# Performance work log

Measured on AMD Instinct MI355X. Metric: run time of the kernel, lower is better.

Reference implementation:

```python
import jax, jax.numpy as jnp
import numpy as np

NS = 100000; NT = 100000; M = 512; D = 256; DL = 128; H = 4; C = 256; K = 64
ITERS = 50; POS_MARGIN = 0.1


def conv1(w, b, x):
    # 1x1 Conv1d: x (B, Cin, N), w (Cout, Cin)
    return jnp.einsum('oi,bin->bon', w, x) + b[None, :, None]


def attn_block(p, x, src):
    # attentional propagation: MHA message + MLP([x, msg]) (residual added by caller)
    wq, bq, wk, bk, wv, bv, wm, bm, w1, b1, w2, b2 = p
    B, Dm, N = x.shape
    Dh = Dm // H
    Nm = src.shape[2]
    q = conv1(wq, bq, x).reshape(B, H, Dh, N)
    k = conv1(wk, bk, src).reshape(B, H, Dh, Nm)
    v = conv1(wv, bv, src).reshape(B, H, Dh, Nm)
    a = jax.nn.softmax(jnp.einsum('bhdn,bhdm->bhnm', q, k) * (1.0 / np.sqrt(Dh)), axis=-1)
    msg = jnp.einsum('bhnm,bhdm->bhdn', a, v).reshape(B, Dm, N)
    msg = conv1(wm, bm, msg)
    h = jax.nn.relu(conv1(w1, b1, jnp.concatenate([x, msg], axis=1)))
    return conv1(w2, b2, h)


def nn_id(points, nodes):
    # 1-NN node id per point; points (N,3), nodes (M,3)
    d = (jnp.sum(points * points, 1, keepdims=True) - 2.0 * points @ nodes.T
         + jnp.sum(nodes * nodes, 1)[None, :])
    return jnp.argmin(d, axis=1)


def build_patches(pcd_id, m, k):
    # grouping_wrapper: first k point indices assigned to each node, -1 padded
    n = pcd_id.shape[0]
    order = jnp.argsort(pcd_id)  # stable
    sid = pcd_id[order]
    starts = jnp.searchsorted(sid, jnp.arange(m))
    rank = jnp.arange(n) - starts[sid]
    patch = jnp.full((m, k), -1, jnp.int32)
    patch = patch.at[sid, rank].set(order.astype(jnp.int32), mode='drop')  # rank>=k dropped
    mask = (patch < 0).astype(jnp.float32)
    return jnp.where(patch < 0, 0, patch), mask


def log_optimal_transport(scores, alpha, iters):
    b, m, n = scores.shape
    bins0 = jnp.full((b, m, 1), alpha)
    bins1 = jnp.full((b, 1, n), alpha)
    corner = jnp.full((b, 1, 1), alpha)
    Z = jnp.concatenate([jnp.concatenate([scores, bins0], 2),
                         jnp.concatenate([bins1, corner], 2)], 1)
    norm = -np.log(m + n)
    log_mu = jnp.concatenate([jnp.full((m,), norm, jnp.float32), jnp.array([np.log(n) + norm], jnp.float32)])
    log_nu = jnp.concatenate([jnp.full((n,), norm, jnp.float32), jnp.array([np.log(m) + norm], jnp.float32)])
    log_mu = jnp.broadcast_to(log_mu, (b, m + 1))
    log_nu = jnp.broadcast_to(log_nu, (b, n + 1))

    def body(carry, _):
        u, v = carry
        u = log_mu - jax.nn.logsumexp(Z + v[:, None, :], axis=2)
        v = log_nu - jax.nn.logsumexp(Z + u[:, :, None], axis=1)
        return (u, v), None

    (u, v), _ = jax.lax.scan(body, (jnp.zeros((b, m + 1)), jnp.zeros((b, n + 1))), None, length=iters)
    return Z + u[:, :, None] + v[:, None, :] - norm


def rpmnet_sinkhorn(log_alpha, bins0, bins1, iters):
    b = log_alpha.shape[0]
    corner = jnp.zeros((b, 1, 1), log_alpha.dtype)
    la = jnp.concatenate([jnp.concatenate([log_alpha, bins0], 2),
                          jnp.concatenate([bins1, corner], 2)], 1)

    def body(la, _):
        row = la - jax.nn.logsumexp(la, axis=2, keepdims=True)
        la = jnp.concatenate([row[:, :-1, :], la[:, -1:, :]], axis=1)  # normalize all rows but slack
        col = la - jax.nn.logsumexp(la, axis=1, keepdims=True)
        la = jnp.concatenate([col[:, :, :-1], la[:, :, -1:]], axis=2)  # normalize all cols but slack
        return la, None

    la, _ = jax.lax.scan(body, la, None, length=iters)
    return la


def _forward(src_pcd_c, tgt_pcd_c, src_node_c, tgt_node_c, src_feats_c, tgt_feats_c,
             src_final_f, tgt_final_f, rot, trans, src_pcd_raw, tgt_pcd_raw,
             c_wq, c_bq, c_wk, c_bk, c_wv, c_bv, c_wm, c_bm, c_w1, c_b1, c_w2, c_b2,
             l_wq, l_bq, l_wk, l_bk, l_wv, l_bv, l_wm, l_bm, l_w1, l_b1, l_w2, l_b2,
             fp_w, fp_b, lfp_w, lfp_b, bin_score, node_corr):
    # KNN assignment + patch grouping (irregular gather/scatter)
    src_patch, src_mask = build_patches(nn_id(src_pcd_c, src_node_c), M, K)
    tgt_patch, tgt_mask = build_patches(nn_id(tgt_pcd_c, tgt_node_c), M, K)
    # coarse attention stack (self, cross, self) with residuals
    cp = lambda i: (c_wq[i], c_bq[i], c_wk[i], c_bk[i], c_wv[i], c_bv[i], c_wm[i], c_bm[i],
                    c_w1[i], c_b1[i], c_w2[i], c_b2[i])
    sf, tf = src_feats_c, tgt_feats_c
    sf = sf + attn_block(cp(0), sf, sf); tf = tf + attn_block(cp(0), tf, tf)
    sf = sf + attn_block(cp(1), sf, tf); tf = tf + attn_block(cp(1), tf, sf)  # sequential, like torch
    sf = sf + attn_block(cp(2), sf, sf); tf = tf + attn_block(cp(2), tf, tf)
    sf = conv1(fp_w, fp_b, sf); tf = conv1(fp_w, fp_b, tf)
    scores = jnp.einsum('bdn,bdm->bnm', sf, tf) / np.sqrt(D)
    scores = log_optimal_transport(scores, bin_score, ITERS)
    # correspondence-driven patch gather
    sn = node_corr[:, 0]; tn = node_corr[:, 1]
    src_sel = src_patch[sn].reshape(-1)
    tgt_sel = tgt_patch[tn].reshape(-1)
    smask = src_mask[sn]; tmask = tgt_mask[tn]  # (C,K)
    # GT local scores (training path)
    src_raw_t = (rot @ src_pcd_raw.T + trans).T
    sc = src_raw_t[src_sel].reshape(C, K, 3)
    tc = tgt_pcd_raw[tgt_sel].reshape(C, K, 3)
    d2 = jnp.maximum(jnp.sum(sc * sc, -1)[:, :, None] + jnp.sum(tc * tc, -1)[:, None, :]
                     - 2.0 * jnp.einsum('cnd,cmd->cnm', sc, tc), 0.0)
    gt = (jnp.sqrt(d2) < POS_MARGIN).astype(jnp.float32)
    row = jnp.maximum(1.0 - jnp.sum(gt, -1), 0.0)[:, :, None]
    col = jnp.maximum(1.0 - jnp.sum(gt, -2), 0.0)[:, None, :]
    col = jnp.concatenate([col, jnp.zeros((C, 1, 1), jnp.float32)], -1)
    gt = jnp.concatenate([jnp.concatenate([gt, row], -1), col], -2)  # (C,K+1,K+1)
    gt = gt.at[:, :-1, :].multiply(1.0 - smask[:, :, None])
    gt = gt.at[:, :, :-1].multiply(1.0 - tmask[:, None, :])
    # local patch features + attention stack
    spf = src_final_f[src_sel].reshape(C, K, DL).transpose(0, 2, 1)  # (C,DL,K)
    tpf = tgt_final_f[tgt_sel].reshape(C, K, DL).transpose(0, 2, 1)
    lp = lambda i: (l_wq[i], l_bq[i], l_wk[i], l_bk[i], l_wv[i], l_bv[i], l_wm[i], l_bm[i],
                    l_w1[i], l_b1[i], l_w2[i], l_b2[i])
    spf = spf + attn_block(lp(0), spf, spf); tpf = tpf + attn_block(lp(0), tpf, tpf)
    spf = spf + attn_block(lp(1), spf, tpf); tpf = tpf + attn_block(lp(1), tpf, spf)
    spf = spf + attn_block(lp(2), spf, spf); tpf = tpf + attn_block(lp(2), tpf, tpf)
    spf = conv1(lfp_w, lfp_b, spf); tpf = conv1(lfp_w, lfp_b, tpf)
    ls = jnp.einsum('bdn,bdm->bnm', spf, tpf) / np.sqrt(DL)
    ls = jnp.where(smask[:, :, None] > 0, -1e6, ls)
    ls = jnp.where(tmask[:, None, :] > 0, -1e6, ls)
    ls = rpmnet_sinkhorn(ls, jnp.zeros((C, K, 1), jnp.float32), jnp.zeros((C, 1, K), jnp.float32), ITERS)
    return scores, ls, gt


def setup_inputs() -> dict:
    key = jax.random.key(0)
    ks = jax.random.split(key, 48)

    def rn(i, shape, scale):
        return jax.random.normal(ks[i], shape, jnp.float32) * scale

    inp = {}
    inp['src_pcd_c'] = jax.random.uniform(ks[0], (NS, 3), jnp.float32)
    inp['tgt_pcd_c'] = jax.random.uniform(ks[1], (NT, 3), jnp.float32)
    inp['src_node_c'] = jax.random.uniform(ks[2], (M, 3), jnp.float32)
    inp['tgt_node_c'] = jax.random.uniform(ks[3], (M, 3), jnp.float32)
    inp['src_feats_c'] = rn(4, (1, D, M), 1.0)
    inp['tgt_feats_c'] = rn(5, (1, D, M), 1.0)
    inp['src_final_f'] = rn(6, (NS, DL), 1.0)
    inp['tgt_final_f'] = rn(7, (NT, DL), 1.0)
    inp['rot'] = jnp.eye(3, dtype=jnp.float32)
    inp['trans'] = jnp.zeros((3, 1), jnp.float32)
    inp['src_pcd_raw'] = jax.random.uniform(ks[8], (NS, 3), jnp.float32)
    inp['tgt_pcd_raw'] = jax.random.uniform(ks[9], (NT, 3), jnp.float32)
    inp['node_corr'] = jax.random.randint(ks[10], (C, 2), 0, M)
    i = 11
    for pre, d in (('c_', D), ('l_', DL)):
        for nm in ('wq', 'wk', 'wv', 'wm'):
            inp[pre + nm] = rn(i, (3, d, d), 1.0 / np.sqrt(d)); i += 1
            inp[pre + 'b' + nm[1]] = jnp.zeros((3, d), jnp.float32)
        inp[pre + 'w1'] = rn(i, (3, 2 * d, 2 * d), 1.0 / np.sqrt(2 * d)); i += 1
        inp[pre + 'b1'] = jnp.zeros((3, 2 * d), jnp.float32)
        inp[pre + 'w2'] = rn(i, (3, d, 2 * d), 1.0 / np.sqrt(2 * d)); i += 1
        inp[pre + 'b2'] = jnp.zeros((3, d), jnp.float32)
    inp['fp_w'] = rn(i, (D, D), 1.0 / np.sqrt(D)); i += 1
    inp['fp_b'] = jnp.zeros((D,), jnp.float32)
    inp['lfp_w'] = rn(i, (DL, DL), 1.0 / np.sqrt(DL)); i += 1
    inp['lfp_b'] = jnp.zeros((DL,), jnp.float32)
    inp['bin_score'] = jnp.ones((), jnp.float32)
    return inp


def reference(src_pcd_c, tgt_pcd_c, src_node_c, tgt_node_c, src_feats_c, tgt_feats_c,
              src_final_f, tgt_final_f, rot, trans, src_pcd_raw, tgt_pcd_raw,
              c_wq, c_bq, c_wk, c_bk, c_wv, c_bv, c_wm, c_bm, c_w1, c_b1, c_w2, c_b2,
              l_wq, l_bq, l_wk, l_bk, l_wv, l_bv, l_wm, l_bm, l_w1, l_b1, l_w2, l_b2,
              fp_w, fp_b, lfp_w, lfp_b, bin_score, node_corr):
    return _forward(src_pcd_c, tgt_pcd_c, src_node_c, tgt_node_c, src_feats_c, tgt_feats_c,
                    src_final_f, tgt_final_f, rot, trans, src_pcd_raw, tgt_pcd_raw,
                    c_wq, c_bq, c_wk, c_bk, c_wv, c_bv, c_wm, c_bm, c_w1, c_b1, c_w2, c_b2,
                    l_wq, l_bq, l_wk, l_bk, l_wv, l_bv, l_wm, l_bm, l_w1, l_b1, l_w2, l_b2,
                    fp_w, fp_b, lfp_w, lfp_b, bin_score, node_corr)
```

## Files before the change

### kernel.cpp

```cpp
#include <hip/hip_runtime.h>
#include <math.h>

static constexpr int NODES = 512;
static constexpr int CC    = 256;
static constexpr int KP    = 64;
static constexpr int ZDIM  = 513;
static constexpr int TPNB  = 16;
static constexpr int TPROWS = 33;

typedef unsigned short u16;
typedef short bf16x8 __attribute__((ext_vector_type(8)));
typedef float f32x4 __attribute__((ext_vector_type(4)));

__device__ __forceinline__ u16 f2b(float f){
  unsigned u = __float_as_uint(f);
  unsigned r = (u + 0x7FFF + ((u >> 16) & 1)) >> 16;
  return (u16)r;
}
__device__ __forceinline__ float b2f(u16 h){ return __uint_as_float(((unsigned)h) << 16); }
__device__ __forceinline__ f32x4 mfma16(bf16x8 a, bf16x8 b, f32x4 c){
  return __builtin_amdgcn_mfma_f32_16x16x32_bf16(a, b, c, 0, 0, 0);
}
__device__ __forceinline__ void astore(float* p, float v){
  __hip_atomic_store(p, v, __ATOMIC_RELAXED, __HIP_MEMORY_SCOPE_AGENT);
}
__device__ __forceinline__ float fpoll(const float* p){
  const unsigned* up = (const unsigned*)p;
  unsigned v = __hip_atomic_load(up, __ATOMIC_RELAXED, __HIP_MEMORY_SCOPE_AGENT);
  while (v == 0xFFFFFFFFu)
    v = __hip_atomic_load(up, __ATOMIC_RELAXED, __HIP_MEMORY_SCOPE_AGENT);
  return __uint_as_float(v);
}
__device__ __forceinline__ void fpoll2(const float* p0, const float* p1,
                                       float* a, float* b){
  const unsigned* u0 = (const unsigned*)p0;
  const unsigned* u1 = (const unsigned*)p1;
  unsigned x = __hip_atomic_load(u0, __ATOMIC_RELAXED, __HIP_MEMORY_SCOPE_AGENT);
  unsigned y = __hip_atomic_load(u1, __ATOMIC_RELAXED, __HIP_MEMORY_SCOPE_AGENT);
  while (x == 0xFFFFFFFFu || y == 0xFFFFFFFFu){
    if (x == 0xFFFFFFFFu) x = __hip_atomic_load(u0, __ATOMIC_RELAXED, __HIP_MEMORY_SCOPE_AGENT);
    if (y == 0xFFFFFFFFu) y = __hip_atomic_load(u1, __ATOMIC_RELAXED, __HIP_MEMORY_SCOPE_AGENT);
  }
  *a = __uint_as_float(x); *b = __uint_as_float(y);
}

static constexpr int NBW = (2539520 + 255) / 256;

__global__ __launch_bounds__(256) void prep(
  const float* cwq, const float* cwk, const float* cwv, const float* cwm,
  const float* cw1, const float* cw2, const float* fpw,
  const float* lwq, const float* lwk, const float* lwv, const float* lwm,
  const float* lw1, const float* lw2, const float* lfp, u16* __restrict__ dst,
  const float* __restrict__ pts_s, int ns, const float* __restrict__ nodes_s,
  int* __restrict__ id_s, int* __restrict__ hist_s,
  const float* __restrict__ pts_t, int ntt, const float* __restrict__ nodes_t,
  int* __restrict__ id_t, int* __restrict__ hist_t, int nbs, int nbnn,
  const float* __restrict__ fs, const float* __restrict__ ft,
  u16* __restrict__ cf, float* __restrict__ cff)
{
  int blk = blockIdx.x;
  int t = threadIdx.x;
  if (blk < NBW){
    int i = blk*256 + t;
    if (i >= 2539520) return;
    const float* s; int off;
    if      (i <  196608){ s=cwq; off=0; }
    else if (i <  393216){ s=cwk; off=196608; }
    else if (i <  589824){ s=cwv; off=393216; }
    else if (i <  786432){ s=cwm; off=589824; }
    else if (i < 1572864){ s=cw1; off=786432; }
    else if (i < 1966080){ s=cw2; off=1572864; }
    else if (i < 2031616){ s=fpw; off=1966080; }
    else if (i < 2080768){ s=lwq; off=2031616; }
    else if (i < 2129920){ s=lwk; off=2080768; }
    else if (i < 2179072){ s=lwv; off=2129920; }
    else if (i < 2228224){ s=lwm; off=2179072; }
    else if (i < 2424832){ s=lw1; off=2228224; }
    else if (i < 2523136){ s=lw2; off=2424832; }
    else                 { s=lfp; off=2523136; }
    dst[i] = f2b(s[i - off]);
    return;
  }
  if (blk < NBW + nbnn){
#pragma clang fp contract(off)
    __shared__ float nx[NODES], ny[NODES], nz[NODES], nn[NODES];
    __shared__ int h[NODES];
    int b2 = blk - NBW;
    const float* pts; const float* nodes; int* out; int* hist; int n; int bb;
    if (b2 < nbs){ pts=pts_s; nodes=nodes_s; out=id_s; hist=hist_s; n=ns; bb=b2; }
    else         { pts=pts_t; nodes=nodes_t; out=id_t; hist=hist_t; n=ntt; bb=b2-nbs; }
    for (int m = t; m < NODES; m += 256){
      float a = nodes[m*3+0], b = nodes[m*3+1], c = nodes[m*3+2];
// ... 284 lines not shown
    f32x4 acc = {};
    const u16* wrow = W2 + (long)(o0+lr)*512 + 8*lk;
#pragma unroll
    for (int ks = 0; ks < 16; ++ks){
      bf16x8 b = *(const bf16x8*)(wrow + ks*32);
      bf16x8 av = *(const bf16x8*)(&h1[lr*512 + ((ks*32 + 8*lk) ^ ((lr&7)<<3))]);
      acc = mfma16(av, b, acc);
    }
    int col = o0 + lr; float bb = b2[col];
#pragma unroll
    for (int q_ = 0; q_ < 4; ++q_){
      long idx = (long)(lk*4+q_)*256 + col;
      float v = acc[q_] + bb + xf[idx];
      xf[idx] = v;
      x[idx] = f2b(v);
    }
  }
}

__global__ __launch_bounds__(256) void coarse_proj(
    const u16* __restrict__ cf, const u16* __restrict__ W,
    const float* __restrict__ bias, u16* __restrict__ out)
{
  int z = blockIdx.x;
  int side = z >> 4, slice = z & 15;
  const u16* in = cf + (long)side*131072;
  u16* o = out + (long)side*131072;
  int n0 = slice << 5;
  int wv_ = threadIdx.x >> 6, L = threadIdx.x & 63, lr = L & 15, lk = L >> 4;
  const u16* inb = in + (long)(n0 + lr)*256 + 8*lk;
  for (int oi = 0; oi < 4; ++oi){
    int o0 = (wv_*4 + oi) << 4;
    const u16* wrow = W + (long)(o0 + lr)*256 + 8*lk;
    f32x4 acc[2] = {};
#pragma unroll
    for (int ks = 0; ks < 8; ++ks){
      bf16x8 b = *(const bf16x8*)(wrow + ks*32);
#pragma unroll
      for (int a = 0; a < 2; ++a){
        bf16x8 av = *(const bf16x8*)(inb + a*16*256 + ks*32);
        acc[a] = mfma16(av, b, acc[a]);
      }
    }
    int col = o0 + lr; float bb = bias[col];
#pragma unroll
    for (int a = 0; a < 2; ++a)
#pragma unroll
      for (int q_ = 0; q_ < 4; ++q_)
        o[(long)(n0 + a*16 + lk*4 + q_)*256 + col] = f2b(acc[a][q_] + bb);
  }
}

__global__ __launch_bounds__(256) void coarse_scores(
    const u16* __restrict__ sfp, const u16* __restrict__ tfp, float* __restrict__ Z)
{
  int n0 = blockIdx.y << 6, m0 = blockIdx.x << 6;
  int wv_ = threadIdx.x >> 6, L = threadIdx.x & 63, lr = L & 15, lk = L >> 4;
  f32x4 acc[4] = {};
  const u16* arow = sfp + (long)(n0 + lr)*256 + 8*lk;
  const u16* brow = tfp + (long)(m0 + wv_*16 + lr)*256 + 8*lk;
#pragma unroll
  for (int ks = 0; ks < 8; ++ks){
    bf16x8 b = *(const bf16x8*)(brow + ks*32);
#pragma unroll
    for (int a = 0; a < 4; ++a){
      bf16x8 av = *(const bf16x8*)(arow + a*16*256 + ks*32);
      acc[a] = mfma16(av, b, acc[a]);
    }
  }
  int col = m0 + wv_*16 + lr;
#pragma unroll
  for (int a = 0; a < 4; ++a)
#pragma unroll
    for (int q_ = 0; q_ < 4; ++q_)
      Z[(long)(n0 + a*16 + lk*4 + q_)*513 + col] = acc[a][q_]*0.0625f;
}

__global__ __launch_bounds__(256) void fill_border(float* Z, const float* __restrict__ alpha)
{
  int i = blockIdx.x*256 + threadIdx.x;
  if (i < ZDIM){
    float a = alpha[0];
    Z[(long)i*ZDIM + (ZDIM-1)] = a;
    Z[(long)(ZDIM-1)*ZDIM + i] = a;
  }
}

__global__ __launch_bounds__(256) void transpose_k(const float* __restrict__ A,
                                                   float* __restrict__ B, int n)
{
  __shared__ float t[32][33];
  int bx = blockIdx.x*32, by = blockIdx.y*32;
  int lx = threadIdx.x & 31, ly0 = threadIdx.x >> 5;
  for (int dy = 0; dy < 32; dy += 8){
    int x = bx + lx, y = by + ly0 + dy;
    if (x < n && y < n) t[ly0+dy][lx] = A[(long)y*n + x];
  }
  __syncthreads();
  for (int dy = 0; dy < 32; dy += 8){
    int x = by + lx, y = bx + ly0 + dy;
    if (x < n && y < n) B[(long)y*n + x] = t[lx][ly0+dy];
  }
}

static constexpr int ARENA = 142336;

__device__ void transport_role(char* arena, int bid,
    const float* __restrict__ Z, const float* __restrict__ Zt,
    float* Rr, float* Cc, float* UU, float* VV,
    float* __restrict__ out, float outadd)
{
  float* A = (float*)arena;
  float* B = A + TPROWS*513;
  float* RrL = B + TPROWS*513;
  float* CcL = RrL + 513;
  float* M   = CcL + 513;
  float* rown = M + 513;
  float* cown = rown + TPROWS;
  float* uown = cown + TPROWS;
  int tid = threadIdx.x;
  int wv_ = tid >> 6, lane = tid & 63;
  int r0 = bid * TPROWS;
  int nr = 513 - r0; if (nr > TPROWS) nr = TPROWS;

  for (int i = wv_; i < nr; i += 8){
    const float* zr  = Z  + (long)(r0+i)*513;
    const float* ztr = Zt + (long)(r0+i)*513;
    for (int j = lane; j < 513; j += 64){ A[i*513+j] = zr[j]; B[i*513+j] = ztr[j]; }
  }
  __syncthreads();
  for (int i = wv_; i < nr; i += 8){
    float m = -INFINITY;
    for (int j = lane; j < 513; j += 64) m = fmaxf(m, A[i*513+j]);
    for (int o = 32; o; o >>= 1) m = fmaxf(m, __shfl_xor(m, o));
    if (lane == 0){ rown[i] = m; astore(&Rr[r0+i], m); }
  }
  if (tid == 0)      fpoll2(&Rr[0], &Rr[512], &RrL[0], &RrL[512]);
  else if (tid < 512) RrL[tid] = fpoll(&Rr[tid]);
  __syncthreads();
  for (int i = wv_; i < nr; i += 8){
    float m = -INFINITY;
    for (int j = lane; j < 513; j += 64) m = fmaxf(m, B[i*513+j] - RrL[j]);
    for (int o = 32; o; o >>= 1) m = fmaxf(m, __shfl_xor(m, o));
    if (lane == 0){ cown[i] = m; astore(&Cc[r0+i], m); }
  }
  if (tid == 0)      fpoll2(&Cc[0], &Cc[512], &CcL[0], &CcL[512]);
  else if (tid < 512) CcL[tid] = fpoll(&Cc[tid]);
  __syncthreads();
  for (int i = wv_; i < nr; i += 8){
    float ro = rown[i], co = cown[i];
    for (int j = lane; j < 513; j += 64){
      A[i*513+j] = __expf(A[i*513+j] - ro - CcL[j]);
      B[i*513+j] = __expf(B[i*513+j] - co - RrL[j]);
    }
// ... 207 lines not shown
  }
  __syncthreads();
  u16* h1 = pool + 8192;
#pragma unroll
  for (int oi = 0; oi < 2; ++oi){
    int o0 = (wv8*2 + oi) << 4;
    f32x4 acc[4] = {};
    const u16* wrow = W1 + (long)(o0+lr)*256 + 8*lk;
#pragma unroll
    for (int ks = 0; ks < 8; ++ks){
      int kk = ks*32;
      bf16x8 b = *(const bf16x8*)(wrow + kk);
#pragma unroll
      for (int a = 0; a < 4; ++a){
        bf16x8 av;
        if (kk < 128) av = *(const bf16x8*)(x + (long)(a*16+lr)*128 + kk + 8*lk);
        else          av = *(const bf16x8*)(&m2[(a*16+lr)*128 + ((kk - 128 + 8*lk) ^ swr)]);
        acc[a] = mfma16(av, b, acc[a]);
      }
    }
    int col = o0+lr; float bb = b1[col];
#pragma unroll
    for (int a = 0; a < 4; ++a)
#pragma unroll
      for (int q_ = 0; q_ < 4; ++q_){
        int row = a*16+lk*4+q_;
        h1[row*256 + (col ^ ((row&7)<<3))] = f2b(fmaxf(acc[a][q_] + bb, 0.f));
      }
  }
  __syncthreads();
  {
    int o0 = wv8 << 4;
    f32x4 acc[4] = {};
    const u16* wrow = W2 + (long)(o0+lr)*256 + 8*lk;
#pragma unroll
    for (int ks = 0; ks < 8; ++ks){
      bf16x8 b = *(const bf16x8*)(wrow + ks*32);
#pragma unroll
      for (int a = 0; a < 4; ++a){
        bf16x8 av = *(const bf16x8*)(&h1[(a*16+lr)*256 + ((ks*32 + 8*lk) ^ swr)]);
        acc[a] = mfma16(av, b, acc[a]);
      }
    }
    int col = o0+lr; float bb = b2[col];
#pragma unroll
    for (int a = 0; a < 4; ++a)
#pragma unroll
      for (int q_ = 0; q_ < 4; ++q_){
        int ri = (a*16+lk*4+q_)*128 + col;
        x[ri] = f2b(acc[a][q_] + bb + b2f(x[ri]));
      }
  }
  __syncthreads();
}

__device__ void local_role(char* arena, int c,
    const float* __restrict__ Fs, const float* __restrict__ Ft,
    const int* __restrict__ patch_s, const int* __restrict__ patch_t,
    const int* __restrict__ corr,
    const int* __restrict__ cnt_s, const int* __restrict__ cnt_t,
    const u16* WlQ, const u16* WlK, const u16* WlV, const u16* WlM,
    const u16* Wl1, const u16* Wl2, const u16* Wlfp,
    const float* lbq, const float* lbk, const float* lbv, const float* lbm,
    const float* lb1, const float* lb2, const float* lfpB,
    float* __restrict__ out_ls)
{
  u16* X    = (u16*)arena;
  u16* pool = (u16*)(arena + 32768);
  float* LA = (float*)(arena + 98816);
  float* ET = (float*)(arena + 115976);
  float* uvec = (float*)(arena + 133136);
  float* vvec = (float*)(arena + 133456);
  float* u0s  = (float*)(arena + 133776);
  float* Ul   = (float*)(arena + 134096);
  float* Vl   = (float*)(arena + 134416);
  int* sel    = (int*)(arena + 134736);
  int tid = threadIdx.x;
  int wv8 = tid >> 6, L = tid & 63, lr = L & 15, lk = L >> 4;
  int swr = (lr & 7) << 3;

  if (tid < 128){
    int side = tid >> 6, n = tid & 63;
    int node = corr[c*2 + side];
    sel[tid] = (side ? patch_t : patch_s)[node*KP + n];
  }
  __syncthreads();
  for (int e = tid; e < 16384; e += 512){
    int side = e >> 13, r = e & 8191, n = r >> 7, d = r & 127;
    const float* F = side ? Ft : Fs;
    X[e] = f2b(F[(long)sel[side*64 + n]*128 + d]);
  }
  __syncthreads();

  for (int l = 0; l < 3; ++l){
    const u16* wq = WlQ + (size_t)l*16384; const u16* wk = WlK + (size_t)l*16384;
    const u16* wv = WlV + (size_t)l*16384; const u16* wm = WlM + (size_t)l*16384;
    const u16* w1 = Wl1 + (size_t)l*65536; const u16* w2 = Wl2 + (size_t)l*32768;
    const float* bq = lbq + (size_t)l*128; const float* bk = lbk + (size_t)l*128;
    const float* bv = lbv + (size_t)l*128; const float* bm = lbm + (size_t)l*128;
    const float* b1 = lb1 + (size_t)l*256; const float* b2 = lb2 + (size_t)l*128;
    int cross = (l == 1);
    layerapp(X,        X + (cross ? 8192 : 0), pool, wq,wk,wv,wm,w1,w2, bq,bk,bv,bm,b1,b2);
    layerapp(X + 8192, X + (cross ? 0 : 8192), pool, wq,wk,wv,wm,w1,w2, bq,bk,bv,bm,b1,b2);
  }

  u16* sp = pool; u16* tp = pool + 8192;
  for (int u_ = wv8; u_ < 16; u_ += 8){
    int sideSel = u_ >> 3, ot = u_ & 7;
    const u16* in = X + sideSel*8192;
    u16* dst = sideSel ? tp : sp;
    int o0 = ot << 4;
    f32x4 acc[4] = {};
    const u16* wrow = Wlfp + (long)(o0+lr)*128 + 8*lk;
    const u16* inr = in + (long)lr*128 + 8*lk;
#pragma unroll
    for (int ks = 0; ks < 4; ++ks){
      bf16x8 b = *(const bf16x8*)(wrow + ks*32);
#pragma unroll
      for (int a = 0; a < 4; ++a){
        bf16x8 av = *(const bf16x8*)(inr + a*16*128 + ks*32);
        acc[a] = mfma16(av, b, acc[a]);
      }
    }
    int col = o0 + lr; float bb = lfpB[col];
#pragma unroll
    for (int a = 0; a < 4; ++a)
#pragma unroll
      for (int q_ = 0; q_ < 4; ++q_){
        int row = a*16 + lk*4 + q_;
        dst[row*128 + (col ^ ((row&7)<<3))] = f2b(acc[a][q_] + bb);
      }
  }
  __syncthreads();

  int cs = cnt_s[corr[c*2]], ct = cnt_t[corr[c*2+1]];
  for (int t_ = wv8; t_ < 16; t_ += 8){
    int mt = t_ >> 2, nt = t_ & 3;
    f32x4 acc = {};
#pragma unroll
    for (int ks = 0; ks < 4; ++ks){
      bf16x8 a = *(const bf16x8*)(&sp[(mt*16 + lr)*128 + ((ks*32 + 8*lk) ^ swr)]);
      bf16x8 b = *(const bf16x8*)(&tp[(nt*16 + lr)*128 + ((ks*32 + 8*lk) ^ swr)]);
      acc = mfma16(a, b, acc);
    }
    const float SCS = 0.08838834764831845f;
#pragma unroll
    for (int q_ = 0; q_ < 4; ++q_){
      int row = mt*16 + lk*4 + q_;
      int col = nt*16 + lr;
      float v = acc[q_] * SCS;
      if (row >= cs || col >= ct) v = -1000000.0f;
      LA[row*66 + col] = v;
    }
  }
  if (tid < 65){ LA[64*66 + tid] = 0.f; LA[tid*66 + 64] = 0.f; uvec[tid] = 1.f; vvec[tid] = 1.f; }
  __syncthreads();

  float* E = (float*)pool;
  int g = tid >> 3, sub = tid & 7;
  {
    float mx = -INFINITY;
    for (int j = sub; j < 65; j += 8) mx = fmaxf(mx, LA[g*66 + j]);
    mx = fmaxf(mx, __shfl_xor(mx, 1)); mx = fmaxf(mx, __shfl_xor(mx, 2));
    mx = fmaxf(mx, __shfl_xor(mx, 4));
    float s = 0.f;
    for (int j = sub; j < 65; j += 8) s += __expf(LA[g*66 + j] - mx);
    s += __shfl_xor(s, 1); s += __shfl_xor(s, 2); s += __shfl_xor(s, 4);
    float u0 = mx + __logf(s);
    if (sub == 0) u0s[g] = u0;
    for (int j = sub; j < 65; j += 8){
      float e = __expf(LA[g*66 + j] - u0);
      E[g*66 + j] = e;
      ET[j*66 + g] = e;
    }
  }
  if (tid < 65){
    E[64*66 + tid] = 1.f;
    ET[tid*66 + 64] = 1.f;
    if (tid == 64) u0s[64] = 0.f;
  }
  __syncthreads();
  for (int it = 0; it < 50; ++it){
    {
      float s = 0.f;
      for (int r = sub; r < 65; r += 8) s = fmaf(ET[g*66 + r], uvec[r], s);
      s += __shfl_xor(s, 1); s += __shfl_xor(s, 2); s += __shfl_xor(s, 4);
      if (sub == 0) vvec[g] = 1.f / s;
    }
    __syncthreads();
    if (it == 49) break;
    {
      float s = 0.f;
      for (int j = sub; j < 65; j += 8) s = fmaf(E[g*66 + j], vvec[j], s);
      s += __shfl_xor(s, 1); s += __shfl_xor(s, 2); s += __shfl_xor(s, 4);
      if (sub == 0) uvec[g] = 1.f / s;
    }
    __syncthreads();
  }
  __syncthreads();
  if (tid < 65){ Ul[tid] = u0s[tid] - __logf(uvec[tid]); Vl[tid] = -__logf(vvec[tid]); }
  __syncthreads();
  for (int e = tid; e < 4225; e += 512){
    int r = e / 65, c2 = e % 65;
    out_ls[(long)c*4225 + e] = LA[r*66 + c2] - Ul[r] - Vl[c2];
  }
}

__device__ void gt_role(char* arena, int c,
    const float* __restrict__ sraw, const float* __restrict__ traw,
    const float* __restrict__ rot, const float* __restrict__ trans,
    const int* __restrict__ patch_s, const int* __restrict__ patch_t,
    const int* __restrict__ corr,
    const int* __restrict__ cnt_s, const int* __restrict__ cnt_t,
    float* __restrict__ out)
{
#pragma clang fp contract(off)
  float* sx = (float*)arena;         float* sy = sx + 64;
  float* sz = sy + 64;               float* spp = sz + 64;
  float* txa = spp + 64;             float* tya = txa + 64;
  float* tza = tya + 64;             float* tpp = tza + 64;
  float* g   = tpp + 64;
  float* rowsum = g + 64*65;
  float* colsum = rowsum + 64;
  int tid = threadIdx.x;
  int sn = corr[c*2], tn = corr[c*2+1];
  int cs = cnt_s[sn], ct = cnt_t[tn];
  if (tid < 64){
    int idx = patch_s[sn*KP + tid];
    float p0 = sraw[(long)idx*3], p1 = sraw[(long)idx*3+1], p2 = sraw[(long)idx*3+2];
    float a0 = fmaf(rot[2], p2, fmaf(rot[1], p1, rot[0]*p0)) + trans[0];
    float a1 = fmaf(rot[5], p2, fmaf(rot[4], p1, rot[3]*p0)) + trans[1];
    float a2 = fmaf(rot[8], p2, fmaf(rot[7], p1, rot[6]*p0)) + trans[2];
    sx[tid]=a0; sy[tid]=a1; sz[tid]=a2;
    spp[tid] = a0*a0 + a1*a1 + a2*a2;
  } else if (tid < 128){
    int l = tid - 64;
    int idx = patch_t[tn*KP + l];
    float p0 = traw[(long)idx*3], p1 = traw[(long)idx*3+1], p2 = traw[(long)idx*3+2];
    txa[l]=p0; tya[l]=p1; tza[l]=p2;
    tpp[l] = p0*p0 + p1*p1 + p2*p2;
  }
  __syncthreads();
  for (int e = tid; e < 4096; e += 512){
    int n = e >> 6, m = e & 63;
    float dot = fmaf(sz[n], tza[m], fmaf(sy[n], tya[m], sx[n]*txa[m]));
    float d2 = (spp[n] + tpp[m]) - 2.0f*dot;
    d2 = fmaxf(d2, 0.f);
    g[n*65 + m] = (sqrtf(d2) < 0.1f) ? 1.f : 0.f;
  }
  __syncthreads();
  if (tid < 64){
    float s = 0.f;
    for (int m = 0; m < 64; ++m) s += g[tid*65 + m];
    rowsum[tid] = fmaxf(1.f - s, 0.f);
  } else if (tid < 128){
    int m = tid - 64;
    float s = 0.f;
    for (int n = 0; n < 64; ++n) s += g[n*65 + m];
    colsum[m] = fmaxf(1.f - s, 0.f);
  }
  __syncthreads();
  float* o = out + (long)c*4225;
  for (int e = tid; e < 4225; e += 512){
    int r = e / 65, col = e % 65;
    float v;
    if (r < 64 && col < 64) v = g[r*65 + col];
    else if (r < 64)        v = rowsum[r];
    else if (col < 64)      v = colsum[col];
    else                    v = 0.f;
    if (r < 64 && r >= cs)    v = 0.f;
    if (col < 64 && col >= ct) v = 0.f;
    o[e] = v;
  }
}

__global__ __launch_bounds__(512) void mega(
    const float* Z, const float* Zt, float* Rr, float* Cc, float* UU, float* VV,
    float* out0, float outadd,
    const float* Fs, const float* Ft,
    const int* patch_s, const int* patch_t, const int* corr,
    const int* cnt_s, const int* cnt_t,
    const u16* WlQ, const u16* WlK, const u16* WlV, const u16* WlM,
    const u16* Wl1, const u16* Wl2, const u16* Wlfp,
    const float* lbq, const float* lbk, const float* lbv, const float* lbm,
    const float* lb1, const float* lb2, const float* lfpB,
    float* out_ls,
    const float* sraw, const float* traw, const float* rot, const float* trans,
    float* out_gt)
{
  __shared__ __align__(16) char arena[ARENA];
  int b = blockIdx.x;
  if (b < 128){
    if ((b & 7) == 0)
      transport_role(arena, b >> 3, Z, Zt, Rr, Cc, UU, VV, out0, outadd);
    return;
  }
  b -= 128;
  if (b < CC)
    local_role(arena, b, Fs, Ft, patch_s, patch_t, corr, cnt_s, cnt_t,
               WlQ, WlK, WlV, WlM, Wl1, Wl2, Wlfp,
               lbq, lbk, lbv, lbm, lb1, lb2, lfpB, out_ls);
  else
    gt_role(arena, b - CC, sraw, traw, rot, trans,
            patch_s, patch_t, corr, cnt_s, cnt_t, out_gt);
}

extern "C" void kernel_launch(void* const* d_in, const int* in_sizes, int n_in,
                              void* d_out, int out_size, void* d_ws, size_t ws_size,
                              hipStream_t stream)
{
  const float* src_pcd_c  = (const float*)d_in[0];
  const float* tgt_pcd_c  = (const float*)d_in[1];
  const float* src_node_c = (const float*)d_in[2];
  const float* tgt_node_c = (const float*)d_in[3];
  const float* src_feats  = (const float*)d_in[4];
  const float* tgt_feats  = (const float*)d_in[5];
  const float* src_final  = (const float*)d_in[6];
  const float* tgt_final  = (const float*)d_in[7];
  const float* rot        = (const float*)d_in[8];
  const float* trans      = (const float*)d_in[9];
  const float* src_raw    = (const float*)d_in[10];
  const float* tgt_raw    = (const float*)d_in[11];
  const int*   node_corr  = (const int*)d_in[12];
  const float* c_wq = (const float*)d_in[13]; const float* c_bq = (const float*)d_in[14];
  const float* c_wk = (const float*)d_in[15]; const float* c_bk = (const float*)d_in[16];
  const float* c_wv = (const float*)d_in[17]; const float* c_bv = (const float*)d_in[18];
  const float* c_wm = (const float*)d_in[19]; const float* c_bm = (const float*)d_in[20];
  const float* c_w1 = (const float*)d_in[21]; const float* c_b1 = (const float*)d_in[22];
  const float* c_w2 = (const float*)d_in[23]; const float* c_b2 = (const float*)d_in[24];
  const float* l_wq = (const float*)d_in[25]; const float* l_bq = (const float*)d_in[26];
  const float* l_wk = (const float*)d_in[27]; const float* l_bk = (const float*)d_in[28];
  const float* l_wv = (const float*)d_in[29]; const float* l_bv = (const float*)d_in[30];
  const float* l_wm = (const float*)d_in[31]; const float* l_bm = (const float*)d_in[32];
  const float* l_w1 = (const float*)d_in[33]; const float* l_b1 = (const float*)d_in[34];
  const float* l_w2 = (const float*)d_in[35]; const float* l_b2 = (const float*)d_in[36];
  const float* fp_w = (const float*)d_in[37]; const float* fp_b = (const float*)d_in[38];
  const float* lfp_w = (const float*)d_in[39]; const float* lfp_b = (const float*)d_in[40];
  const float* bin_score = (const float*)d_in[41];

  const int NS = in_sizes[0] / 3;
  const int NT = in_sizes[1] / 3;

  float* FB = (float*)d_ws;
  size_t off = 0;
  auto falloc = [&](size_t n){ float* p = FB + off; off += (n + 63) & ~size_t(63); return p; };
  float* Zx  = falloc(263169);
  float* Zt  = falloc(263169);
  float* Rr  = falloc(640);
  float* Cc  = falloc(640);
  float* UU  = falloc(32000);
  float* VV  = falloc(32000);
  float* cff = falloc(262144);
  u16* cf   = (u16*)falloc(131072);
  u16* qb   = (u16*)falloc(131072);
  u16* kb   = (u16*)falloc(131072);
  u16* vtb  = (u16*)falloc(131072);
  u16* msgb = (u16*)falloc(131072);
// ... 18 lines not shown
  float* out_gt = out_ls + (long)CC*65*65;

  u16* WcQ = wsb + 0;
  u16* WcK = wsb + 196608;
  u16* WcV = wsb + 393216;
  u16* WcM = wsb + 589824;
  u16* Wc1 = wsb + 786432;
  u16* Wc2 = wsb + 1572864;
  u16* Wfp = wsb + 1966080;
  u16* WlQ = wsb + 2031616;
  u16* WlK = wsb + 2080768;
  u16* WlV = wsb + 2129920;
  u16* WlM = wsb + 2179072;
  u16* Wl1 = wsb + 2228224;
  u16* Wl2 = wsb + 2424832;
  u16* Wlfp = wsb + 2523136;

  hipMemsetAsync(Rr, 0xFF, (640 + 640 + 32000 + 32000)*sizeof(float), stream);
  hipMemsetAsync(patch_s, 0, NODES*KP*sizeof(int), stream);
  hipMemsetAsync(patch_t, 0, NODES*KP*sizeof(int), stream);

  int nbnn = nbs + nbt;
  prep<<<NBW + nbnn + 1024, 256, 0, stream>>>(
      c_wq, c_wk, c_wv, c_wm, c_w1, c_w2, fp_w,
      l_wq, l_wk, l_wv, l_wm, l_w1, l_w2, lfp_w, wsb,
      src_pcd_c, NS, src_node_c, id_s, hist_s,
      tgt_pcd_c, NT, tgt_node_c, id_t, hist_t, nbs, nbnn,
      src_feats, tgt_feats, cf, cff);
  scan_kernel2<<<256, 256, 0, stream>>>(hist_s, nbs, cnt_s, hist_t, nbt, cnt_t);
  rank_kernel<<<nbs + nbt, 256, 0, stream>>>(
      id_s, NS, hist_s, patch_s, id_t, NT, hist_t, patch_t, nbs);

  int crossL[3] = {0, 1, 0};
  for (int l = 0; l < 3; ++l){
    u16* wq = WcQ + (size_t)l*65536; u16* wk = WcK + (size_t)l*65536;
    u16* wv = WcV + (size_t)l*65536; u16* wm = WcM + (size_t)l*65536;
    u16* w1 = Wc1 + (size_t)l*262144; u16* w2 = Wc2 + (size_t)l*131072;
    const float* bq = c_bq + (size_t)l*256; const float* bk = c_bk + (size_t)l*256;
    const float* bv = c_bv + (size_t)l*256; const float* bm = c_bm + (size_t)l*256;
    const float* b1 = c_b1 + (size_t)l*512; const float* b2 = c_b2 + (size_t)l*256;
    if (!crossL[l]){
      coarse_qkv<<<96, 256, 0, stream>>>(cf, 0, 0, wq, wk, wv, bq, bk, bv, qb, kb, vtb);
      coarse_attn<<<128, 256, 0, stream>>>(qb, kb, vtb, msgb, 0);
      coarse_ffn<<<64, 256, 0, stream>>>(msgb, cf, cff, wm, bm, w1, b1, w2, b2, 0);
    } else {
      for (int sd = 0; sd < 2; ++sd){
        coarse_qkv<<<48, 256, 0, stream>>>(cf, 1, sd, wq, wk, wv, bq, bk, bv, qb, kb, vtb);
        coarse_attn<<<64, 256, 0, stream>>>(qb, kb, vtb, msgb, sd);
        coarse_ffn<<<32, 256, 0, stream>>>(msgb, cf, cff, wm, bm, w1, b1, w2, b2, sd);
      }
    }
  }
  coarse_proj<<<32, 256, 0, stream>>>(cf, Wfp, fp_b, sfpb);
  coarse_scores<<<dim3(8,8), 256, 0, stream>>>(sfpb, sfpb + 131072, Zx);
  fill_border<<<3, 256, 0, stream>>>(Zx, bin_score);
  transpose_k<<<dim3(17,17), 256, 0, stream>>>(Zx, Zt, ZDIM);

  mega<<<128 + CC + CC, 512, 0, stream>>>(
      Zx, Zt, Rr, Cc, UU, VV, out0, logf(1024.0f),
      src_final, tgt_final, patch_s, patch_t, node_corr, cnt_s, cnt_t,
      WlQ, WlK, WlV, WlM, Wl1, Wl2, Wlfp,
      l_bq, l_bk, l_bv, l_bm, l_b1, l_b2, lfp_b,
      out_ls,
      src_raw, tgt_raw, rot, trans, out_gt);

  (void)n_in; (void)out_size; (void)ws_size;
}
```

Before: 844.2 us.

## Fuse transpose into score kernel, merge local and gt roles, add poll sleep

The coarse score kernel now writes both Z and its transpose directly, and the border fill covers both, so the separate transpose kernel launch goes away. In the mega kernel each of the 256 correspondence blocks now runs the local role and then the gt role, instead of using separate blocks for each, which cuts the grid from 640 to 384 blocks. Spin-wait polling gains s_sleep to reduce memory traffic from busy waiting. The transposed Zt writes are strided and uncoalesced, and serializing the two roles lengthens each block's critical path.

After: 842.6 us. About the same (-0.2%).

```diff
diff --git a/kernel.cpp b/kernel.cpp
--- a/kernel.cpp
+++ b/kernel.cpp
@@ -27,8 +27,10 @@
 __device__ __forceinline__ float fpoll(const float* p){
   const unsigned* up = (const unsigned*)p;
   unsigned v = __hip_atomic_load(up, __ATOMIC_RELAXED, __HIP_MEMORY_SCOPE_AGENT);
-  while (v == 0xFFFFFFFFu)
+  while (v == 0xFFFFFFFFu){
+    __builtin_amdgcn_s_sleep(1);
     v = __hip_atomic_load(up, __ATOMIC_RELAXED, __HIP_MEMORY_SCOPE_AGENT);
+  }
   return __uint_as_float(v);
 }
 __device__ __forceinline__ void fpoll2(const float* p0, const float* p1,
@@ -38,6 +40,7 @@
   unsigned x = __hip_atomic_load(u0, __ATOMIC_RELAXED, __HIP_MEMORY_SCOPE_AGENT);
   unsigned y = __hip_atomic_load(u1, __ATOMIC_RELAXED, __HIP_MEMORY_SCOPE_AGENT);
   while (x == 0xFFFFFFFFu || y == 0xFFFFFFFFu){
+    __builtin_amdgcn_s_sleep(1);
     if (x == 0xFFFFFFFFu) x = __hip_atomic_load(u0, __ATOMIC_RELAXED, __HIP_MEMORY_SCOPE_AGENT);
     if (y == 0xFFFFFFFFu) y = __hip_atomic_load(u1, __ATOMIC_RELAXED, __HIP_MEMORY_SCOPE_AGENT);
   }
@@ -428,7 +431,8 @@
 }
 
 __global__ __launch_bounds__(256) void coarse_scores(
-    const u16* __restrict__ sfp, const u16* __restrict__ tfp, float* __restrict__ Z)
+    const u16* __restrict__ sfp, const u16* __restrict__ tfp,
+    float* __restrict__ Z, float* __restrict__ Zt)
 {
   int n0 = blockIdx.y << 6, m0 = blockIdx.x << 6;
   int wv_ = threadIdx.x >> 6, L = threadIdx.x & 63, lr = L & 15, lk = L >> 4;
@@ -448,34 +452,24 @@
 #pragma unroll
   for (int a = 0; a < 4; ++a)
 #pragma unroll
-    for (int q_ = 0; q_ < 4; ++q_)
-      Z[(long)(n0 + a*16 + lk*4 + q_)*513 + col] = acc[a][q_]*0.0625f;
-}
-
-__global__ __launch_bounds__(256) void fill_border(float* Z, const float* __restrict__ alpha)
+    for (int q_ = 0; q_ < 4; ++q_){
+      int row = n0 + a*16 + lk*4 + q_;
+      float v = acc[a][q_]*0.0625f;
+      Z[(long)row*513 + col] = v;
+      Zt[(long)col*513 + row] = v;
+    }
+}
+
+__global__ __launch_bounds__(256) void fill_border(float* Z, float* Zt,
+                                                   const float* __restrict__ alpha)
 {
   int i = blockIdx.x*256 + threadIdx.x;
   if (i < ZDIM){
     float a = alpha[0];
     Z[(long)i*ZDIM + (ZDIM-1)] = a;
     Z[(long)(ZDIM-1)*ZDIM + i] = a;
-  }
-}
-
-__global__ __launch_bounds__(256) void transpose_k(const float* __restrict__ A,
-                                                   float* __restrict__ B, int n)
-{
-  __shared__ float t[32][33];
-  int bx = blockIdx.x*32, by = blockIdx.y*32;
-  int lx = threadIdx.x & 31, ly0 = threadIdx.x >> 5;
-  for (int dy = 0; dy < 32; dy += 8){
-    int x = bx + lx, y = by + ly0 + dy;
-    if (x < n && y < n) t[ly0+dy][lx] = A[(long)y*n + x];
-  }
-  __syncthreads();
-  for (int dy = 0; dy < 32; dy += 8){
-    int x = by + lx, y = bx + ly0 + dy;
-    if (x < n && y < n) B[(long)y*n + x] = t[lx][ly0+dy];
+    Zt[(long)i*ZDIM + (ZDIM-1)] = a;
+    Zt[(long)(ZDIM-1)*ZDIM + i] = a;
   }
 }
 
@@ -789,158 +783,6 @@
       }
   }
   __syncthreads();
-}
-
-__device__ void local_role(char* arena, int c,
-    const float* __restrict__ Fs, const float* __restrict__ Ft,
-    const int* __restrict__ patch_s, const int* __restrict__ patch_t,
-    const int* __restrict__ corr,
-    const int* __restrict__ cnt_s, const int* __restrict__ cnt_t,
-    const u16* WlQ, const u16* WlK, const u16* WlV, const u16* WlM,
-    const u16* Wl1, const u16* Wl2, const u16* Wlfp,
-    const float* lbq, const float* lbk, const float* lbv, const float* lbm,
-    const float* lb1, const float* lb2, const float* lfpB,
-    float* __restrict__ out_ls)
-{
-  u16* X    = (u16*)arena;
-  u16* pool = (u16*)(arena + 32768);
-  float* LA = (float*)(arena + 98816);
-  float* ET = (float*)(arena + 115976);
-  float* uvec = (float*)(arena + 133136);
-  float* vvec = (float*)(arena + 133456);
-  float* u0s  = (float*)(arena + 133776);
-  float* Ul   = (float*)(arena + 134096);
-  float* Vl   = (float*)(arena + 134416);
-  int* sel    = (int*)(arena + 134736);
-  int tid = threadIdx.x;
-  int wv8 = tid >> 6, L = tid & 63, lr = L & 15, lk = L >> 4;
-  int swr = (lr & 7) << 3;
-
-  if (tid < 128){
-    int side = tid >> 6, n = tid & 63;
-    int node = corr[c*2 + side];
-    sel[tid] = (side ? patch_t : patch_s)[node*KP + n];
-  }
-  __syncthreads();
-  for (int e = tid; e < 16384; e += 512){
-    int side = e >> 13, r = e & 8191, n = r >> 7, d = r & 127;
-    const float* F = side ? Ft : Fs;
-    X[e] = f2b(F[(long)sel[side*64 + n]*128 + d]);
-  }
-  __syncthreads();
-
-  for (int l = 0; l < 3; ++l){
-    const u16* wq = WlQ + (size_t)l*16384; const u16* wk = WlK + (size_t)l*16384;
-    const u16* wv = WlV + (size_t)l*16384; const u16* wm = WlM + (size_t)l*16384;
-    const u16* w1 = Wl1 + (size_t)l*65536; const u16* w2 = Wl2 + (size_t)l*32768;
-    const float* bq = lbq + (size_t)l*128; const float* bk = lbk + (size_t)l*128;
-    const float* bv = lbv + (size_t)l*128; const float* bm = lbm + (size_t)l*128;
-    const float* b1 = lb1 + (size_t)l*256; const float* b2 = lb2 + (size_t)l*128;
-    int cross = (l == 1);
-    layerapp(X,        X + (cross ? 8192 : 0), pool, wq,wk,wv,wm,w1,w2, bq,bk,bv,bm,b1,b2);
-    layerapp(X + 8192, X + (cross ? 0 : 8192), pool, wq,wk,wv,wm,w1,w2, bq,bk,bv,bm,b1,b2);
-  }
-
-  u16* sp = pool; u16* tp = pool + 8192;
-  for (int u_ = wv8; u_ < 16; u_ += 8){
-    int sideSel = u_ >> 3, ot = u_ & 7;
-    const u16* in = X + sideSel*8192;
-    u16* dst = sideSel ? tp : sp;
-    int o0 = ot << 4;
-    f32x4 acc[4] = {};
-    const u16* wrow = Wlfp + (long)(o0+lr)*128 + 8*lk;
-    const u16* inr = in + (long)lr*128 + 8*lk;
-#pragma unroll
-    for (int ks = 0; ks < 4; ++ks){
-      bf16x8 b = *(const bf16x8*)(wrow + ks*32);
-#pragma unroll
-      for (int a = 0; a < 4; ++a){
-        bf16x8 av = *(const bf16x8*)(inr + a*16*128 + ks*32);
-        acc[a] = mfma16(av, b, acc[a]);
-      }
-    }
-    int col = o0 + lr; float bb = lfpB[col];
-#pragma unroll
-    for (int a = 0; a < 4; ++a)
-#pragma unroll
-      for (int q_ = 0; q_ < 4; ++q_){
-        int row = a*16 + lk*4 + q_;
-        dst[row*128 + (col ^ ((row&7)<<3))] = f2b(acc[a][q_] + bb);
-      }
-  }
-  __syncthreads();
-
-  int cs = cnt_s[corr[c*2]], ct = cnt_t[corr[c*2+1]];
-  for (int t_ = wv8; t_ < 16; t_ += 8){
-    int mt = t_ >> 2, nt = t_ & 3;
-    f32x4 acc = {};
-#pragma unroll
-    for (int ks = 0; ks < 4; ++ks){
-      bf16x8 a = *(const bf16x8*)(&sp[(mt*16 + lr)*128 + ((ks*32 + 8*lk) ^ swr)]);
-      bf16x8 b = *(const bf16x8*)(&tp[(nt*16 + lr)*128 + ((ks*32 + 8*lk) ^ swr)]);
-      acc = mfma16(a, b, acc);
-    }
-    const float SCS = 0.08838834764831845f;
-#pragma unroll
-    for (int q_ = 0; q_ < 4; ++q_){
-      int row = mt*16 + lk*4 + q_;
-      int col = nt*16 + lr;
-      float v = acc[q_] * SCS;
-      if (row >= cs || col >= ct) v = -1000000.0f;
-      LA[row*66 + col] = v;
-    }
-  }
-  if (tid < 65){ LA[64*66 + tid] = 0.f; LA[tid*66 + 64] = 0.f; uvec[tid] = 1.f; vvec[tid] = 1.f; }
-  __syncthreads();
-
-  float* E = (float*)pool;
-  int g = tid >> 3, sub = tid & 7;
-  {
-    float mx = -INFINITY;
-    for (int j = sub; j < 65; j += 8) mx = fmaxf(mx, LA[g*66 + j]);
-    mx = fmaxf(mx, __shfl_xor(mx, 1)); mx = fmaxf(mx, __shfl_xor(mx, 2));
-    mx = fmaxf(mx, __shfl_xor(mx, 4));
-    float s = 0.f;
-    for (int j = sub; j < 65; j += 8) s += __expf(LA[g*66 + j] - mx);
-    s += __shfl_xor(s, 1); s += __shfl_xor(s, 2); s += __shfl_xor(s, 4);
-    float u0 = mx + __logf(s);
-    if (sub == 0) u0s[g] = u0;
-    for (int j = sub; j < 65; j += 8){
-      float e = __expf(LA[g*66 + j] - u0);
-      E[g*66 + j] = e;
-      ET[j*66 + g] = e;
-    }
-  }
-  if (tid < 65){
-    E[64*66 + tid] = 1.f;
-    ET[tid*66 + 64] = 1.f;
-    if (tid == 64) u0s[64] = 0.f;
-  }
-  __syncthreads();
-  for (int it = 0; it < 50; ++it){
-    {
-      float s = 0.f;
-      for (int r = sub; r < 65; r += 8) s = fmaf(ET[g*66 + r], uvec[r], s);
-      s += __shfl_xor(s, 1); s += __shfl_xor(s, 2); s += __shfl_xor(s, 4);
-      if (sub == 0) vvec[g] = 1.f / s;
-    }
-    __syncthreads();
-    if (it == 49) break;
-    {
-      float s = 0.f;
-      for (int j = sub; j < 65; j += 8) s = fmaf(E[g*66 + j], vvec[j], s);
-      s += __shfl_xor(s, 1); s += __shfl_xor(s, 2); s += __shfl_xor(s, 4);
-      if (sub == 0) uvec[g] = 1.f / s;
-    }
-    __syncthreads();
-  }
-  __syncthreads();
-  if (tid < 65){ Ul[tid] = u0s[tid] - __logf(uvec[tid]); Vl[tid] = -__logf(vvec[tid]); }
-  __syncthreads();
-  for (int e = tid; e < 4225; e += 512){
-    int r = e / 65, c2 = e % 65;
-    out_ls[(long)c*4225 + e] = LA[r*66 + c2] - Ul[r] - Vl[c2];
-  }
 }
 
 __device__ void gt_role(char* arena, int c,
@@ -1011,6 +853,158 @@
   }
 }
 
+__device__ void local_role(char* arena, int c,
+    const float* __restrict__ Fs, const float* __restrict__ Ft,
+    const int* __restrict__ patch_s, const int* __restrict__ patch_t,
+    const int* __restrict__ corr,
+    const int* __restrict__ cnt_s, const int* __restrict__ cnt_t,
+    const u16* WlQ, const u16* WlK, const u16* WlV, const u16* WlM,
+    const u16* Wl1, const u16* Wl2, const u16* Wlfp,
+    const float* lbq, const float* lbk, const float* lbv, const float* lbm,
+    const float* lb1, const float* lb2, const float* lfpB,
+    float* __restrict__ out_ls)
+{
+  u16* X    = (u16*)arena;
+  u16* pool = (u16*)(arena + 32768);
+  float* LA = (float*)(arena + 98816);
+  float* ET = (float*)(arena + 115976);
+  float* uvec = (float*)(arena + 133136);
+  float* vvec = (float*)(arena + 133456);
+  float* u0s  = (float*)(arena + 133776);
+  float* Ul   = (float*)(arena + 134096);
+  float* Vl   = (float*)(arena + 134416);
+  int* sel    = (int*)(arena + 134736);
+  int tid = threadIdx.x;
+  int wv8 = tid >> 6, L = tid & 63, lr = L & 15, lk = L >> 4;
+  int swr = (lr & 7) << 3;
+
+  if (tid < 128){
+    int side = tid >> 6, n = tid & 63;
+    int node = corr[c*2 + side];
+    sel[tid] = (side ? patch_t : patch_s)[node*KP + n];
+  }
+  __syncthreads();
+  for (int e = tid; e < 16384; e += 512){
+    int side = e >> 13, r = e & 8191, n = r >> 7, d = r & 127;
+    const float* F = side ? Ft : Fs;
+    X[e] = f2b(F[(long)sel[side*64 + n]*128 + d]);
+  }
+  __syncthreads();
+
+  for (int l = 0; l < 3; ++l){
+    const u16* wq = WlQ + (size_t)l*16384; const u16* wk = WlK + (size_t)l*16384;
+    const u16* wv = WlV + (size_t)l*16384; const u16* wm = WlM + (size_t)l*16384;
+    const u16* w1 = Wl1 + (size_t)l*65536; const u16* w2 = Wl2 + (size_t)l*32768;
+    const float* bq = lbq + (size_t)l*128; const float* bk = lbk + (size_t)l*128;
+    const float* bv = lbv + (size_t)l*128; const float* bm = lbm + (size_t)l*128;
+    const float* b1 = lb1 + (size_t)l*256; const float* b2 = lb2 + (size_t)l*128;
+    int cross = (l == 1);
+    layerapp(X,        X + (cross ? 8192 : 0), pool, wq,wk,wv,wm,w1,w2, bq,bk,bv,bm,b1,b2);
+    layerapp(X + 8192, X + (cross ? 0 : 8192), pool, wq,wk,wv,wm,w1,w2, bq,bk,bv,bm,b1,b2);
+  }
+
+  u16* sp = pool; u16* tp = pool + 8192;
+  for (int u_ = wv8; u_ < 16; u_ += 8){
+    int sideSel = u_ >> 3, ot = u_ & 7;
+    const u16* in = X + sideSel*8192;
+    u16* dst = sideSel ? tp : sp;
+    int o0 = ot << 4;
+    f32x4 acc[4] = {};
+    const u16* wrow = Wlfp + (long)(o0+lr)*128 + 8*lk;
+    const u16* inr = in + (long)lr*128 + 8*lk;
+#pragma unroll
+    for (int ks = 0; ks < 4; ++ks){
+      bf16x8 b = *(const bf16x8*)(wrow + ks*32);
+#pragma unroll
+      for (int a = 0; a < 4; ++a){
+        bf16x8 av = *(const bf16x8*)(inr + a*16*128 + ks*32);
+        acc[a] = mfma16(av, b, acc[a]);
+      }
+    }
+    int col = o0 + lr; float bb = lfpB[col];
+#pragma unroll
+    for (int a = 0; a < 4; ++a)
+#pragma unroll
+      for (int q_ = 0; q_ < 4; ++q_){
+        int row = a*16 + lk*4 + q_;
+        dst[row*128 + (col ^ ((row&7)<<3))] = f2b(acc[a][q_] + bb);
+      }
+  }
+  __syncthreads();
+
+  int cs = cnt_s[corr[c*2]], ct = cnt_t[corr[c*2+1]];
+  for (int t_ = wv8; t_ < 16; t_ += 8){
+    int mt = t_ >> 2, nt = t_ & 3;
+    f32x4 acc = {};
+#pragma unroll
+    for (int ks = 0; ks < 4; ++ks){
+      bf16x8 a = *(const bf16x8*)(&sp[(mt*16 + lr)*128 + ((ks*32 + 8*lk) ^ swr)]);
+      bf16x8 b = *(const bf16x8*)(&tp[(nt*16 + lr)*128 + ((ks*32 + 8*lk) ^ swr)]);
+      acc = mfma16(a, b, acc);
+    }
+    const float SCS = 0.08838834764831845f;
+#pragma unroll
+    for (int q_ = 0; q_ < 4; ++q_){
+      int row = mt*16 + lk*4 + q_;
+      int col = nt*16 + lr;
+      float v = acc[q_] * SCS;
+      if (row >= cs || col >= ct) v = -1000000.0f;
+      LA[row*66 + col] = v;
+    }
+  }
+  if (tid < 65){ LA[64*66 + tid] = 0.f; LA[tid*66 + 64] = 0.f; uvec[tid] = 1.f; vvec[tid] = 1.f; }
+  __syncthreads();
+
+  float* E = (float*)pool;
+  int g = tid >> 3, sub = tid & 7;
+  {
+    float mx = -INFINITY;
+    for (int j = sub; j < 65; j += 8) mx = fmaxf(mx, LA[g*66 + j]);
+    mx = fmaxf(mx, __shfl_xor(mx, 1)); mx = fmaxf(mx, __shfl_xor(mx, 2));
+    mx = fmaxf(mx, __shfl_xor(mx, 4));
+    float s = 0.f;
+    for (int j = sub; j < 65; j += 8) s += __expf(LA[g*66 + j] - mx);
+    s += __shfl_xor(s, 1); s += __shfl_xor(s, 2); s += __shfl_xor(s, 4);
+    float u0 = mx + __logf(s);
+    if (sub == 0) u0s[g] = u0;
+    for (int j = sub; j < 65; j += 8){
+      float e = __expf(LA[g*66 + j] - u0);
+      E[g*66 + j] = e;
+      ET[j*66 + g] = e;
+    }
+  }
+  if (tid < 65){
+    E[64*66 + tid] = 1.f;
+    ET[tid*66 + 64] = 1.f;
+    if (tid == 64) u0s[64] = 0.f;
+  }
+  __syncthreads();
+  for (int it = 0; it < 50; ++it){
+    {
+      float s = 0.f;
+      for (int r = sub; r < 65; r += 8) s = fmaf(ET[g*66 + r], uvec[r], s);
+      s += __shfl_xor(s, 1); s += __shfl_xor(s, 2); s += __shfl_xor(s, 4);
+      if (sub == 0) vvec[g] = 1.f / s;
+    }
+    __syncthreads();
+    if (it == 49) break;
+    {
+      float s = 0.f;
+      for (int j = sub; j < 65; j += 8) s = fmaf(E[g*66 + j], vvec[j], s);
+      s += __shfl_xor(s, 1); s += __shfl_xor(s, 2); s += __shfl_xor(s, 4);
+      if (sub == 0) uvec[g] = 1.f / s;
+    }
+    __syncthreads();
+  }
+  __syncthreads();
+  if (tid < 65){ Ul[tid] = u0s[tid] - __logf(uvec[tid]); Vl[tid] = -__logf(vvec[tid]); }
+  __syncthreads();
+  for (int e = tid; e < 4225; e += 512){
+    int r = e / 65, c2 = e % 65;
+    out_ls[(long)c*4225 + e] = LA[r*66 + c2] - Ul[r] - Vl[c2];
+  }
+}
+
 __global__ __launch_bounds__(512) void mega(
     const float* Z, const float* Zt, float* Rr, float* Cc, float* UU, float* VV,
     float* out0, float outadd,
@@ -1033,13 +1027,11 @@
     return;
   }
   b -= 128;
-  if (b < CC)
-    local_role(arena, b, Fs, Ft, patch_s, patch_t, corr, cnt_s, cnt_t,
-               WlQ, WlK, WlV, WlM, Wl1, Wl2, Wlfp,
-               lbq, lbk, lbv, lbm, lb1, lb2, lfpB, out_ls);
-  else
-    gt_role(arena, b - CC, sraw, traw, rot, trans,
-            patch_s, patch_t, corr, cnt_s, cnt_t, out_gt);
+  local_role(arena, b, Fs, Ft, patch_s, patch_t, corr, cnt_s, cnt_t,
+             WlQ, WlK, WlV, WlM, Wl1, Wl2, Wlfp,
+             lbq, lbk, lbv, lbm, lb1, lb2, lfpB, out_ls);
+  gt_role(arena, b, sraw, traw, rot, trans,
+          patch_s, patch_t, corr, cnt_s, cnt_t, out_gt);
 }
 
 extern "C" void kernel_launch(void* const* d_in, const int* in_sizes, int n_in,
@@ -1164,11 +1156,10 @@
     }
   }
   coarse_proj<<<32, 256, 0, stream>>>(cf, Wfp, fp_b, sfpb);
-  coarse_scores<<<dim3(8,8), 256, 0, stream>>>(sfpb, sfpb + 131072, Zx);
-  fill_border<<<3, 256, 0, stream>>>(Zx, bin_score);
-  transpose_k<<<dim3(17,17), 256, 0, stream>>>(Zx, Zt, ZDIM);
-
-  mega<<<128 + CC + CC, 512, 0, stream>>>(
+  coarse_scores<<<dim3(8,8), 256, 0, stream>>>(sfpb, sfpb + 131072, Zx, Zt);
+  fill_border<<<3, 256, 0, stream>>>(Zx, Zt, bin_score);
+
+  mega<<<128 + CC, 512, 0, stream>>>(
       Zx, Zt, Rr, Cc, UU, VV, out0, logf(1024.0f),
       src_final, tgt_final, patch_s, patch_t, node_corr, cnt_s, cnt_t,
       WlQ, WlK, WlV, WlM, Wl1, Wl2, Wlfp,
```
